# Performance work log

Hardware: AMD Instinct MI355X
Metric: run time of the kernel (lower is better)

The kernel has to match this reference:

```python
import jax, jax.numpy as jnp
import numpy as np

S = 0.7071067811865476  # 1/sqrt(2), pywt haar filter coefficient
# For output j=2k the source coord is k-0.25 (frac 0.75), for j=2k+1 it is k+0.25 (frac 0.25).
_WE = (-0.03515625, 0.26171875, 0.87890625, -0.10546875)  # even outputs, taps at k-2..k+1


def haar_dwt2(x):
    # pywt wavedec2 single level with 'haar': cA=(x0+x1)/sqrt2, cD=(x0-x1)/sqrt2 per pair
    a = (x[..., ::2] + x[..., 1::2]) * S
    d = (x[..., ::2] - x[..., 1::2]) * S
    aa = (a[..., ::2, :] + a[..., 1::2, :]) * S   # LL
    da = (a[..., ::2, :] - a[..., 1::2, :]) * S   # cH (LH)
    ad = (d[..., ::2, :] + d[..., 1::2, :]) * S   # cV (HL)
    dd = (d[..., ::2, :] - d[..., 1::2, :]) * S   # cD (HH)
    return aa, da, ad, dd


def _interleave(e, o, axis):
    stacked = jnp.stack([e, o], axis=axis)
    shp = list(e.shape)
    shp[axis] *= 2
    return stacked.reshape(shp)


def haar_idwt2(aa, da, ad, dd):
    # invert columns (axis -2): x0=(a+d)/sqrt2, x1=(a-d)/sqrt2
    a = _interleave((aa + da) * S, (aa - da) * S, -2)
    d = _interleave((ad + dd) * S, (ad - dd) * S, -2)
    return _interleave((a + d) * S, (a - d) * S, -1)


def area_down2(x):
    h, w = x.shape[-2] // 2, x.shape[-1] // 2
    return x.reshape(*x.shape[:-2], h, 2, w, 2).mean(axis=(-3, -1))


def _up2_last(x):
    n = x.shape[-1]
    p = jnp.pad(x, [(0, 0)] * (x.ndim - 1) + [(2, 2)], mode='edge')  # replicate border like cv2
    ev = (_WE[0] * p[..., 0:n] + _WE[1] * p[..., 1:n + 1]
          + _WE[2] * p[..., 2:n + 2] + _WE[3] * p[..., 3:n + 3])
    od = (_WE[3] * p[..., 1:n + 1] + _WE[2] * p[..., 2:n + 2]
          + _WE[1] * p[..., 3:n + 3] + _WE[0] * p[..., 4:n + 4])
    return jnp.stack([ev, od], axis=-1).reshape(*x.shape[:-1], 2 * n)


def cubic_up2(x):
    x = _up2_last(x)
    return jnp.swapaxes(_up2_last(jnp.swapaxes(x, -1, -2)), -1, -2)


def dwt_roundtrip(x):
    B, C, H, W = x.shape
    # ---- encode ----
    aa1, lh1, hl1, hh1 = haar_dwt2(x)          # level 1: [B,C,H/2,W/2]
    ll2, lh2, hl2, hh2 = haar_dwt2(aa1)        # level 2: [B,C,H/4,W/4]
    bands = jnp.stack([ll2, lh2, hl2, hh2,
                       area_down2(lh1), area_down2(hl1), area_down2(hh1)], axis=2)
    z = bands.reshape(B, C * 7, H // 4, W // 4)
    # ---- decode ----
    b = z.reshape(B, C, 7, H // 4, W // 4)
    lh1u = cubic_up2(b[:, :, 4])
    hl1u = cubic_up2(b[:, :, 5])
    hh1u = cubic_up2(b[:, :, 6])
    aa1r = haar_idwt2(b[:, :, 0], b[:, :, 1], b[:, :, 2], b[:, :, 3])
    return haar_idwt2(aa1r, lh1u, hl1u, hh1u)


def setup_inputs() -> dict:
    key = jax.random.key(0)
    x = jax.random.normal(key, (32, 3, 512, 512), dtype=jnp.float32)
    return {"x": x}


def reference(x):
    return dwt_roundtrip(x)
```

## Files before the change

### kernel.cpp

```cpp
#include <hip/hip_runtime.h>


#define WE0 (-0.03515625f)
#define WE1 (0.26171875f)
#define WE2 (0.87890625f)
#define WE3 (-0.10546875f)

__global__ __launch_bounds__(256) void dwt_fused_kernel(
    const float* __restrict__ x, float* __restrict__ out)
{
    __shared__ float dband[3][36][36];
    __shared__ float aaT[64][66];

    const int tid  = threadIdx.x;
    const int b    = blockIdx.x;
    const int bc   = b >> 4;
    const int tile = b & 15;
    const int tr   = tile >> 2;
    const int tc   = tile & 3;

    const float* xp = x + ((size_t)bc << 18);
    float* op       = out + ((size_t)bc << 18);

    const int bdr = tr * 32 - 2;
    const int bdc = tc * 32 - 2;

    for (int task = tid; task < 36 * 36; task += 256) {
        const int i = task / 36;
        const int j = task - 36 * i;
        const int dr = min(max(bdr + i, 0), 127);
        const int dc = min(max(bdc + j, 0), 127);

        float v[4][4];
#pragma unroll
        for (int r = 0; r < 4; ++r) {
            const float4 rv = *reinterpret_cast<const float4*>(
                xp + (size_t)(4 * dr + r) * 512 + 4 * dc);
            v[r][0] = rv.x; v[r][1] = rv.y; v[r][2] = rv.z; v[r][3] = rv.w;
        }

        float aa[2][2];
        float lhs = 0.f, hls = 0.f, hhs = 0.f;
#pragma unroll
        for (int sr = 0; sr < 2; ++sr) {
#pragma unroll
            for (int sc = 0; sc < 2; ++sc) {
                const float x00 = v[2*sr][2*sc],   x01 = v[2*sr][2*sc+1];
                const float x10 = v[2*sr+1][2*sc], x11 = v[2*sr+1][2*sc+1];
                aa[sr][sc] = 0.5f * (x00 + x01 + x10 + x11);
                lhs += 0.5f * (x00 + x01 - x10 - x11);
                hls += 0.5f * (x00 - x01 + x10 - x11);
                hhs += 0.5f * (x00 - x01 - x10 + x11);
            }
        }

        dband[0][i][j] = 0.25f * lhs;
        dband[1][i][j] = 0.25f * hls;
        dband[2][i][j] = 0.25f * hhs;

        if ((unsigned)(i - 2) < 32u && (unsigned)(j - 2) < 32u) {
            const int ar = 2 * (i - 2), ac = 2 * (j - 2);
            aaT[ar][ac]     = aa[0][0];
            aaT[ar][ac + 1] = aa[0][1];
            aaT[ar + 1][ac]     = aa[1][0];
            aaT[ar + 1][ac + 1] = aa[1][1];
        }
    }

    __syncthreads();

    for (int blk = tid; blk < 1024; blk += 256) {
        const int kr = blk >> 5;
        const int kc = blk & 31;

        float U[3][2][2];
#pragma unroll
        for (int bb = 0; bb < 3; ++bb) {
            float he[5], ho[5];
#pragma unroll
            for (int i = 0; i < 5; ++i) {
                const float* rowp = &dband[bb][kr + i][kc];
                const float d0 = rowp[0], d1 = rowp[1], d2 = rowp[2],
                            d3 = rowp[3], d4 = rowp[4];
                he[i] = WE0 * d0 + WE1 * d1 + WE2 * d2 + WE3 * d3;
                ho[i] = WE3 * d1 + WE2 * d2 + WE1 * d3 + WE0 * d4;
            }
            U[bb][0][0] = WE0*he[0] + WE1*he[1] + WE2*he[2] + WE3*he[3];
            U[bb][0][1] = WE0*ho[0] + WE1*ho[1] + WE2*ho[2] + WE3*ho[3];
            U[bb][1][0] = WE3*he[1] + WE2*he[2] + WE1*he[3] + WE0*he[4];
            U[bb][1][1] = WE3*ho[1] + WE2*ho[2] + WE1*ho[3] + WE0*ho[4];
        }

        const int orow = tr * 128 + 4 * kr;
        const int ocol = tc * 128 + 4 * kc;
#pragma unroll
        for (int i = 0; i < 2; ++i) {
            const float a0 = aaT[2*kr + i][2*kc];
            const float a1 = aaT[2*kr + i][2*kc + 1];
            float o0[4], o1[4];
#pragma unroll
            for (int j = 0; j < 2; ++j) {
                const float aaV = (j == 0) ? a0 : a1;
                const float da = U[0][i][j], ad = U[1][i][j], dd = U[2][i][j];
                const float s1 = aaV + da, t1 = aaV - da;
                const float s2 = ad + dd,  t2 = ad - dd;
                o0[2*j]     = 0.5f * (s1 + s2);
                o0[2*j + 1] = 0.5f * (s1 - s2);
                o1[2*j]     = 0.5f * (t1 + t2);
                o1[2*j + 1] = 0.5f * (t1 - t2);
            }
            *reinterpret_cast<float4*>(op + (size_t)(orow + 2*i) * 512 + ocol) =
                make_float4(o0[0], o0[1], o0[2], o0[3]);
            *reinterpret_cast<float4*>(op + (size_t)(orow + 2*i + 1) * 512 + ocol) =
                make_float4(o1[0], o1[1], o1[2], o1[3]);
        }
    }
}

extern "C" void kernel_launch(void* const* d_in, const int* in_sizes, int n_in,
                              void* d_out, int out_size, void* d_ws, size_t ws_size,
                              hipStream_t stream)
{
    const float* x = (const float*)d_in[0];
    float* out = (float*)d_out;
    (void)d_ws; (void)ws_size;

    const int blocks = 96 * 16;
    dwt_fused_kernel<<<blocks, 256, 0, stream>>>(x, out);
}
```

Baseline: 184.9 us.

## Widen blocks, swizzle block order, pad LDS, vectorize, and use nontemporal stores

Raises the block to 512 threads with launch bounds (512, 8) and swizzles the block index so consecutive blocks land on different image planes. Pads the shared-memory arrays and reads them with vector loads. Each thread now computes two output column groups, sharing the horizontal cubic taps through accumulated vertical filtering. Output is written with nontemporal 16-byte stores to skip cache pollution. The kernel is memory-bound and moves about 400MB, so gains depend on DRAM efficiency; the larger blocks and occupancy target could add register pressure.

```diff
diff --git a/kernel.cpp b/kernel.cpp
--- a/kernel.cpp
+++ b/kernel.cpp
@@ -6,18 +6,20 @@
 #define WE2 (0.87890625f)
 #define WE3 (-0.10546875f)
 
-__global__ __launch_bounds__(256) void dwt_fused_kernel(
+typedef float v4f __attribute__((ext_vector_type(4)));
+typedef float v2f __attribute__((ext_vector_type(2)));
+
+__global__ __launch_bounds__(512, 8) void dwt_fused_kernel(
     const float* __restrict__ x, float* __restrict__ out)
 {
-    __shared__ float dband[3][36][36];
-    __shared__ float aaT[64][66];
+    __shared__ float db[3][36][40];
+    __shared__ float aaT[64][68];
 
-    const int tid  = threadIdx.x;
-    const int b    = blockIdx.x;
-    const int bc   = b >> 4;
-    const int tile = b & 15;
-    const int tr   = tile >> 2;
-    const int tc   = tile & 3;
+    const int tid = threadIdx.x;
+    const int swz  = (blockIdx.x & 7) * 192 + (blockIdx.x >> 3);
+    const int bc   = swz >> 4;
+    const int tile = swz & 15;
+    const int tr = tile >> 2, tc = tile & 3;
 
     const float* xp = x + ((size_t)bc << 18);
     float* op       = out + ((size_t)bc << 18);
@@ -25,95 +27,119 @@
     const int bdr = tr * 32 - 2;
     const int bdc = tc * 32 - 2;
 
-    for (int task = tid; task < 36 * 36; task += 256) {
+    for (int task = tid; task < 1296; task += 512) {
         const int i = task / 36;
         const int j = task - 36 * i;
         const int dr = min(max(bdr + i, 0), 127);
         const int dc = min(max(bdc + j, 0), 127);
 
-        float v[4][4];
-#pragma unroll
-        for (int r = 0; r < 4; ++r) {
-            const float4 rv = *reinterpret_cast<const float4*>(
-                xp + (size_t)(4 * dr + r) * 512 + 4 * dc);
-            v[r][0] = rv.x; v[r][1] = rv.y; v[r][2] = rv.z; v[r][3] = rv.w;
-        }
+        const float* src = xp + (size_t)(4 * dr) * 512 + 4 * dc;
+        const v4f r0 = *reinterpret_cast<const v4f*>(src);
+        const v4f r1 = *reinterpret_cast<const v4f*>(src + 512);
+        const v4f r2 = *reinterpret_cast<const v4f*>(src + 1024);
+        const v4f r3 = *reinterpret_cast<const v4f*>(src + 1536);
 
-        float aa[2][2];
-        float lhs = 0.f, hls = 0.f, hhs = 0.f;
-#pragma unroll
-        for (int sr = 0; sr < 2; ++sr) {
-#pragma unroll
-            for (int sc = 0; sc < 2; ++sc) {
-                const float x00 = v[2*sr][2*sc],   x01 = v[2*sr][2*sc+1];
-                const float x10 = v[2*sr+1][2*sc], x11 = v[2*sr+1][2*sc+1];
-                aa[sr][sc] = 0.5f * (x00 + x01 + x10 + x11);
-                lhs += 0.5f * (x00 + x01 - x10 - x11);
-                hls += 0.5f * (x00 - x01 + x10 - x11);
-                hhs += 0.5f * (x00 - x01 - x10 + x11);
-            }
-        }
+        const float aa00 = 0.5f * (r0.x + r0.y + r1.x + r1.y);
+        const float aa01 = 0.5f * (r0.z + r0.w + r1.z + r1.w);
+        const float aa10 = 0.5f * (r2.x + r2.y + r3.x + r3.y);
+        const float aa11 = 0.5f * (r2.z + r2.w + r3.z + r3.w);
+        const float lhs = (r0.x + r0.y - r1.x - r1.y) + (r0.z + r0.w - r1.z - r1.w)
+                        + (r2.x + r2.y - r3.x - r3.y) + (r2.z + r2.w - r3.z - r3.w);
+        const float hls = (r0.x - r0.y + r1.x - r1.y) + (r0.z - r0.w + r1.z - r1.w)
+                        + (r2.x - r2.y + r3.x - r3.y) + (r2.z - r2.w + r3.z - r3.w);
+        const float hhs = (r0.x - r0.y - r1.x + r1.y) + (r0.z - r0.w - r1.z + r1.w)
+                        + (r2.x - r2.y - r3.x + r3.y) + (r2.z - r2.w - r3.z + r3.w);
 
-        dband[0][i][j] = 0.25f * lhs;
-        dband[1][i][j] = 0.25f * hls;
-        dband[2][i][j] = 0.25f * hhs;
+        db[0][i][j] = 0.125f * lhs;
+        db[1][i][j] = 0.125f * hls;
+        db[2][i][j] = 0.125f * hhs;
 
         if ((unsigned)(i - 2) < 32u && (unsigned)(j - 2) < 32u) {
             const int ar = 2 * (i - 2), ac = 2 * (j - 2);
-            aaT[ar][ac]     = aa[0][0];
-            aaT[ar][ac + 1] = aa[0][1];
-            aaT[ar + 1][ac]     = aa[1][0];
-            aaT[ar + 1][ac + 1] = aa[1][1];
+            *reinterpret_cast<v2f*>(&aaT[ar][ac])     = (v2f){ aa00, aa01 };
+            *reinterpret_cast<v2f*>(&aaT[ar + 1][ac]) = (v2f){ aa10, aa11 };
         }
     }
 
     __syncthreads();
 
-    for (int blk = tid; blk < 1024; blk += 256) {
-        const int kr = blk >> 5;
-        const int kc = blk & 31;
+    const int kr = tid >> 4;
+    const int c  = tid & 15;
+    const int kc0 = 2 * c;
 
-        float U[3][2][2];
+    float U[3][2][2][2];
 #pragma unroll
-        for (int bb = 0; bb < 3; ++bb) {
-            float he[5], ho[5];
+    for (int b = 0; b < 3; ++b)
 #pragma unroll
-            for (int i = 0; i < 5; ++i) {
-                const float* rowp = &dband[bb][kr + i][kc];
-                const float d0 = rowp[0], d1 = rowp[1], d2 = rowp[2],
-                            d3 = rowp[3], d4 = rowp[4];
-                he[i] = WE0 * d0 + WE1 * d1 + WE2 * d2 + WE3 * d3;
-                ho[i] = WE3 * d1 + WE2 * d2 + WE1 * d3 + WE0 * d4;
+        for (int i = 0; i < 2; ++i)
+#pragma unroll
+            for (int p = 0; p < 2; ++p)
+                U[b][i][p][0] = U[b][i][p][1] = 0.f;
+
+    constexpr float WEv[4] = { WE0, WE1, WE2, WE3 };
+
+#pragma unroll
+    for (int b = 0; b < 3; ++b) {
+#pragma unroll
+        for (int r = 0; r < 5; ++r) {
+            const float* rp = &db[b][kr + r][kc0];
+            const v2f w01 = *reinterpret_cast<const v2f*>(rp);
+            const v2f w23 = *reinterpret_cast<const v2f*>(rp + 2);
+            const v2f w45 = *reinterpret_cast<const v2f*>(rp + 4);
+            const float he0 = WE0*w01.x + WE1*w01.y + WE2*w23.x + WE3*w23.y;
+            const float ho0 = WE3*w01.y + WE2*w23.x + WE1*w23.y + WE0*w45.x;
+            const float he1 = WE0*w01.y + WE1*w23.x + WE2*w23.y + WE3*w45.x;
+            const float ho1 = WE3*w23.x + WE2*w23.y + WE1*w45.x + WE0*w45.y;
+            if (r < 4) {
+                const float wv = WEv[r];
+                U[b][0][0][0] += wv * he0;  U[b][0][0][1] += wv * ho0;
+                U[b][0][1][0] += wv * he1;  U[b][0][1][1] += wv * ho1;
             }
-            U[bb][0][0] = WE0*he[0] + WE1*he[1] + WE2*he[2] + WE3*he[3];
-            U[bb][0][1] = WE0*ho[0] + WE1*ho[1] + WE2*ho[2] + WE3*ho[3];
-            U[bb][1][0] = WE3*he[1] + WE2*he[2] + WE1*he[3] + WE0*he[4];
-            U[bb][1][1] = WE3*ho[1] + WE2*ho[2] + WE1*ho[3] + WE0*ho[4];
+            if (r > 0) {
+                const float wv = WEv[4 - r];
+                U[b][1][0][0] += wv * he0;  U[b][1][0][1] += wv * ho0;
+                U[b][1][1][0] += wv * he1;  U[b][1][1][1] += wv * ho1;
+            }
         }
+    }
 
-        const int orow = tr * 128 + 4 * kr;
-        const int ocol = tc * 128 + 4 * kc;
+    const v4f aar0 = *reinterpret_cast<const v4f*>(&aaT[2 * kr][4 * c]);
+    const v4f aar1 = *reinterpret_cast<const v4f*>(&aaT[2 * kr + 1][4 * c]);
+    const float aav[2][4] = { { aar0.x, aar0.y, aar0.z, aar0.w },
+                              { aar1.x, aar1.y, aar1.z, aar1.w } };
+
+    const int orow0 = tr * 128 + 4 * kr;
+    const int ocol  = tc * 128 + 8 * c;
+
 #pragma unroll
-        for (int i = 0; i < 2; ++i) {
-            const float a0 = aaT[2*kr + i][2*kc];
-            const float a1 = aaT[2*kr + i][2*kc + 1];
-            float o0[4], o1[4];
+    for (int i = 0; i < 2; ++i) {
+        float otop[8], obot[8];
+#pragma unroll
+        for (int p = 0; p < 2; ++p) {
 #pragma unroll
             for (int j = 0; j < 2; ++j) {
-                const float aaV = (j == 0) ? a0 : a1;
-                const float da = U[0][i][j], ad = U[1][i][j], dd = U[2][i][j];
+                const float aaV = aav[i][2 * p + j];
+                const float da = U[0][i][p][j];
+                const float ad = U[1][i][p][j];
+                const float dd = U[2][i][p][j];
                 const float s1 = aaV + da, t1 = aaV - da;
                 const float s2 = ad + dd,  t2 = ad - dd;
-                o0[2*j]     = 0.5f * (s1 + s2);
-                o0[2*j + 1] = 0.5f * (s1 - s2);
-                o1[2*j]     = 0.5f * (t1 + t2);
-                o1[2*j + 1] = 0.5f * (t1 - t2);
+                otop[4*p + 2*j]     = 0.5f * (s1 + s2);
+                otop[4*p + 2*j + 1] = 0.5f * (s1 - s2);
+                obot[4*p + 2*j]     = 0.5f * (t1 + t2);
+                obot[4*p + 2*j + 1] = 0.5f * (t1 - t2);
             }
-            *reinterpret_cast<float4*>(op + (size_t)(orow + 2*i) * 512 + ocol) =
-                make_float4(o0[0], o0[1], o0[2], o0[3]);
-            *reinterpret_cast<float4*>(op + (size_t)(orow + 2*i + 1) * 512 + ocol) =
-                make_float4(o1[0], o1[1], o1[2], o1[3]);
         }
+        float* rt = op + (size_t)(orow0 + 2 * i) * 512 + ocol;
+        float* rb = rt + 512;
+        __builtin_nontemporal_store((v4f){otop[0], otop[1], otop[2], otop[3]},
+                                    reinterpret_cast<v4f*>(rt));
+        __builtin_nontemporal_store((v4f){otop[4], otop[5], otop[6], otop[7]},
+                                    reinterpret_cast<v4f*>(rt + 4));
+        __builtin_nontemporal_store((v4f){obot[0], obot[1], obot[2], obot[3]},
+                                    reinterpret_cast<v4f*>(rb));
+        __builtin_nontemporal_store((v4f){obot[4], obot[5], obot[6], obot[7]},
+                                    reinterpret_cast<v4f*>(rb + 4));
     }
 }
 
@@ -126,5 +152,5 @@
     (void)d_ws; (void)ws_size;
 
     const int blocks = 96 * 16;
-    dwt_fused_kernel<<<blocks, 256, 0, stream>>>(x, out);
+    dwt_fused_kernel<<<blocks, 512, 0, stream>>>(x, out);
 }
```

Result: slower. 206.0 us (+11.4%).
